# Kernel optimization log

Hardware: AMD Instinct MI355X
Metric: run time of the kernel (lower is better)

The kernel has to match this reference:

```python
import jax, jax.numpy as jnp
import numpy as np

NUM_ITER = 5
ALPHA = 5.0   # spatial bandwidth, bilateral kernel
BETA = 5.0    # feature bandwidth, bilateral kernel
GAMMA = 5.0   # spatial bandwidth, spatial kernel
W_1 = 1.0
W_2 = 1.0


def setup_inputs() -> dict:
    key = jax.random.key(0)
    k1, k2 = jax.random.split(key)
    B, C, X, Y, Z = 1, 4, 32, 16, 16
    log_unary = jax.random.normal(k1, (B, C, X, Y, Z), dtype=jnp.float32)
    features_pairwise = jax.random.normal(k2, (B, 2, X, Y, Z), dtype=jnp.float32)
    # Potts-model compatibility: ones minus identity, [C_out, C_in] (conv1d kernel size 1)
    compatibility_weights = (jnp.ones((C, C)) - jnp.eye(C)).astype(jnp.float32)
    return {"log_unary": log_unary, "features_pairwise": features_pairwise,
            "compatibility_weights": compatibility_weights}


def _gauss_kernel(f):
    # f: [B, D, N] feature vectors; dense Gaussian filter matrix K_ij = exp(-||f_i-f_j||^2/2)
    sq = jnp.sum(f * f, axis=1)  # [B, N]
    d2 = sq[:, :, None] + sq[:, None, :] - 2.0 * jnp.einsum('bdn,bdm->bnm', f, f)
    return jnp.exp(-0.5 * jnp.maximum(d2, 0.0))  # [B, N, N]


def reference(log_unary, features_pairwise, compatibility_weights):
    B, C, X, Y, Z = log_unary.shape
    N = X * Y * Z
    lu = log_unary.reshape(B, C, N)
    q = jax.nn.softmax(lu, axis=1)

    gx, gy, gz = jnp.meshgrid(jnp.arange(X), jnp.arange(Y), jnp.arange(Z), indexing='ij')
    spatial = jnp.stack([gx, gy, gz], axis=0).astype(jnp.float32).reshape(1, 3, N)
    spatial = jnp.broadcast_to(spatial, (B, 3, N))
    img_fea = features_pairwise.reshape(B, features_pairwise.shape[1], N)

    f1 = jnp.concatenate([spatial / ALPHA, img_fea / BETA], axis=1)  # bilateral features
    f2 = spatial / GAMMA                                             # spatial features

    K1 = _gauss_kernel(f1)
    K2 = _gauss_kernel(f2)
    # norm = filter(ones) = row sums; scale = rsqrt(norm)
    scale1 = jax.lax.rsqrt(jnp.sum(K1, axis=2))[:, None, :]  # [B,1,N]
    scale2 = jax.lax.rsqrt(jnp.sum(K2, axis=2))[:, None, :]

    for _ in range(NUM_ITER):
        q1 = jnp.einsum('bnm,bcm->bcn', K1, q * scale1) * scale1
        q2 = jnp.einsum('bnm,bcm->bcn', K2, q * scale2) * scale2
        q_comb = W_1 * q1 + W_2 * q2
        q_update = jnp.einsum('oc,bcn->bon', compatibility_weights, q_comb)
        q = jax.nn.softmax(lu - q_update, axis=1)

    return q.reshape(B, C, X, Y, Z)
```

## Files before the change

### kernel.cpp

```cpp
#include <hip/hip_runtime.h>
#include <math.h>


constexpr int   NT    = 8192;
constexpr float SQL2E = 1.2011224087864498f;
constexpr float LOG2E = 1.4426950408889634f;
constexpr float INVA  = 0.2f * SQL2E;

constexpr int R_M = 0, R_U1 = 32, R_U2 = 36, R_S1 = 40, R_S2 = 41, R_CV = 42;

static __device__ __forceinline__ float ex2(float x) {
    return __builtin_amdgcn_exp2f(x);
}

__constant__ float INVSQF[7] = {1.f, 1.f, 0.70710678f, 0.40824829f,
                                0.20412415f, 0.09128709f, 0.03726780f};

__global__ __launch_bounds__(256) void k_setup(const float* __restrict__ feat,
                                               float* __restrict__ W) {
    int n = blockIdx.x * 256 + threadIdx.x;
    float g0 = feat[n] * 0.2f, g1 = feat[NT + n] * 0.2f;
    float eg = ex2(-0.5f * LOG2E * (g0*g0 + g1*g1));
    float p0[7], p1[7];
    p0[0] = 1.f; p1[0] = 1.f;
#pragma unroll
    for (int i = 1; i < 7; i++) { p0[i] = p0[i-1]*g0; p1[i] = p1[i-1]*g1; }
    int ab = 0;
#pragma unroll
    for (int k = 0; k <= 6; k++)
#pragma unroll
        for (int a = k; a >= 0; a--) {
            int b = k - a;
            W[(R_M + ab)*NT + n] = eg * p0[a]*INVSQF[a] * p1[b]*INVSQF[b];
            ab++;
        }
    int x = n >> 8, y = (n >> 4) & 15, z = n & 15;
    float Sx = 0.f, Sy = 0.f, Sz = 0.f;
    for (int j = 0; j < 32; j++) { float d = (float)(x-j)*INVA; Sx += ex2(-0.5f*d*d); }
    for (int j = 0; j < 16; j++) { float d = (float)(y-j)*INVA; Sy += ex2(-0.5f*d*d); }
    for (int j = 0; j < 16; j++) { float d = (float)(z-j)*INVA; Sz += ex2(-0.5f*d*d); }
    W[R_S2*NT + n] = rsqrtf(Sx * Sy * Sz);
}

__global__ __launch_bounds__(256) void k_conv(const float* __restrict__ W,
                                              float* __restrict__ Wout, int mode) {
    __shared__ float SP[512 * 17];
    const int idx = blockIdx.x;
    const int tid = threadIdx.x;
    if (mode == 0) {
        const float* src = W + (R_M + idx) * NT;
        for (int s = tid; s < NT; s += 256)
            SP[(s >> 4)*17 + (s & 15)] = src[s];
    } else if (idx < 112) {
        const float* Mr = W + (R_M + (idx >> 2)) * NT;
        const float* ur = W + (R_U1 + (idx & 3)) * NT;
        for (int s = tid; s < NT; s += 256)
            SP[(s >> 4)*17 + (s & 15)] = Mr[s] * ur[s];
    } else {
        const float* ur = W + (R_U2 + (idx - 112)) * NT;
        for (int s = tid; s < NT; s += 256)
            SP[(s >> 4)*17 + (s & 15)] = ur[s];
    }
    float g32[32];
#pragma unroll
    for (int d = 0; d < 32; d++) { float t = d * INVA; g32[d] = ex2(-0.5f*t*t); }
    __syncthreads();
#pragma unroll
    for (int rr = 0; rr < 2; rr++) {
        int r = tid + rr * 256;
        float v[16], acc[16];
#pragma unroll
        for (int z = 0; z < 16; z++) { v[z] = SP[r*17 + z]; acc[z] = 0.f; }
#pragma unroll
        for (int zp = 0; zp < 16; zp++)
#pragma unroll
            for (int z = 0; z < 16; z++) {
                int d = (z > zp) ? (z - zp) : (zp - z);
                acc[z] = fmaf(g32[d], v[zp], acc[z]);
            }
#pragma unroll
        for (int z = 0; z < 16; z++) SP[r*17 + z] = acc[z];
    }
    __syncthreads();
#pragma unroll
    for (int rr = 0; rr < 2; rr++) {
        int r = tid + rr * 256;
        int x = r >> 4, z = r & 15;
        int base = x * 272 + z;
        float v[16], acc[16];
#pragma unroll
        for (int y = 0; y < 16; y++) { v[y] = SP[base + y*17]; acc[y] = 0.f; }
#pragma unroll
        for (int yp = 0; yp < 16; yp++)
#pragma unroll
            for (int y = 0; y < 16; y++) {
                int d = (y > yp) ? (y - yp) : (yp - y);
                acc[y] = fmaf(g32[d], v[yp], acc[y]);
            }
#pragma unroll
        for (int y = 0; y < 16; y++) SP[base + y*17] = acc[y];
    }
    __syncthreads();
    {
        int base = (tid >> 4) * 17 + (tid & 15);
        float v[32], acc[32];
#pragma unroll
        for (int xp = 0; xp < 32; xp++) { v[xp] = SP[base + xp*272]; acc[xp] = 0.f; }
#pragma unroll
        for (int xp = 0; xp < 32; xp++)
#pragma unroll
            for (int x = 0; x < 32; x++) {
                int d = (x > xp) ? (x - xp) : (xp - x);
                acc[x] = fmaf(g32[d], v[xp], acc[x]);
            }
        float* outp = Wout + (R_CV + idx) * NT;
#pragma unroll
        for (int x = 0; x < 32; x++) outp[x*256 + tid] = acc[x];
    }
}

__global__ __launch_bounds__(256) void k_init(float* __restrict__ W,
                                              const float* __restrict__ lu) {
    int n = blockIdx.x * 256 + threadIdx.x;
    float rs = 0.f;
#pragma unroll
    for (int ab = 0; ab < 28; ab++)
        rs = fmaf(W[(R_M+ab)*NT + n], W[(R_CV+ab)*NT + n], rs);
    float s1 = rsqrtf(rs);
    float s2 = W[R_S2*NT + n];
    W[R_S1*NT + n] = s1;
    float l0 = lu[n], l1 = lu[NT+n], l2 = lu[2*NT+n], l3 = lu[3*NT+n];
    float mx = fmaxf(fmaxf(l0,l1), fmaxf(l2,l3));
    float q0 = __expf(l0-mx), q1 = __expf(l1-mx), q2 = __expf(l2-mx), q3 = __expf(l3-mx);
    float inv = 1.f / (q0+q1+q2+q3);
    q0*=inv; q1*=inv; q2*=inv; q3*=inv;
    W[(R_U1+0)*NT+n]=q0*s1; W[(R_U1+1)*NT+n]=q1*s1; W[(R_U1+2)*NT+n]=q2*s1; W[(R_U1+3)*NT+n]=q3*s1;
    W[(R_U2+0)*NT+n]=q0*s2; W[(R_U2+1)*NT+n]=q1*s2; W[(R_U2+2)*NT+n]=q2*s2; W[(R_U2+3)*NT+n]=q3*s2;
}

__global__ __launch_bounds__(256) void k_fuse(float* __restrict__ W,
        const float* __restrict__ lu, const float* __restrict__ compat,
        float* __restrict__ out) {
    int n = blockIdx.x * 256 + threadIdx.x;
    float s1 = W[R_S1*NT + n], s2 = W[R_S2*NT + n];
    float q1[4] = {0.f, 0.f, 0.f, 0.f};
#pragma unroll
    for (int ab = 0; ab < 28; ab++) {
        float m = W[(R_M+ab)*NT + n];
#pragma unroll
        for (int c = 0; c < 4; c++)
            q1[c] = fmaf(m, W[(R_CV + ab*4 + c)*NT + n], q1[c]);
    }
    float comb[4];
#pragma unroll
    for (int c = 0; c < 4; c++)
        comb[c] = s1 * q1[c] + s2 * W[(R_CV + 112 + c)*NT + n];
    float q[4];
#pragma unroll
    for (int o = 0; o < 4; o++) {
        float upd = 0.f;
#pragma unroll
        for (int c = 0; c < 4; c++) upd = fmaf(compat[o*4+c], comb[c], upd);
        q[o] = lu[o*NT+n] - upd;
    }
    float mx = fmaxf(fmaxf(q[0],q[1]), fmaxf(q[2],q[3]));
    float sum = 0.f;
#pragma unroll
    for (int c = 0; c < 4; c++) { q[c] = __expf(q[c]-mx); sum += q[c]; }
    float inv = 1.f / sum;
#pragma unroll
    for (int c = 0; c < 4; c++) {
        q[c] *= inv;
        out[c*NT+n]        = q[c];
        W[(R_U1+c)*NT+n]   = q[c]*s1;
        W[(R_U2+c)*NT+n]   = q[c]*s2;
    }
}

extern "C" void kernel_launch(void* const* d_in, const int* in_sizes, int n_in,
                              void* d_out, int out_size, void* d_ws, size_t ws_size,
                              hipStream_t stream) {
    const float* lu     = (const float*)d_in[0];
    const float* feat   = (const float*)d_in[1];
    const float* compat = (const float*)d_in[2];
    float* out = (float*)d_out;
    float* W   = (float*)d_ws;

    k_setup<<<dim3(32), dim3(256), 0, stream>>>(feat, W);
    k_conv <<<dim3(28), dim3(256), 0, stream>>>(W, W, 0);
    k_init <<<dim3(32), dim3(256), 0, stream>>>(W, lu);
    for (int it = 0; it < 5; it++) {
        k_conv<<<dim3(116), dim3(256), 0, stream>>>(W, W, 1);
        k_fuse<<<dim3(32),  dim3(256), 0, stream>>>(W, lu, compat, out);
    }
}
```

Before: 147.2 us.

## Fuse all stages into one persistent kernel with atomic grid barriers

Replaces the thirteen separate kernel launches (setup, initial conv, init, then conv+fuse per iteration) with a single persistent kernel of 116 blocks that synchronises stages through an atomic-counter grid barrier. Setup is folded into the first conv stage by computing the moment channels directly into shared memory, and the final iteration skips writing the scaled q buffers. This is meant to remove per-launch overhead and inter-kernel gaps. In exchange it adds a memset launch, spin-wait barriers that depend on all 116 blocks being co-resident, and extra atomic latency at each stage boundary.

```diff
diff --git a/kernel.cpp b/kernel.cpp
--- a/kernel.cpp
+++ b/kernel.cpp
@@ -3,68 +3,35 @@
 
 
 constexpr int   NT    = 8192;
+constexpr int   NB    = 116;
 constexpr float SQL2E = 1.2011224087864498f;
 constexpr float LOG2E = 1.4426950408889634f;
 constexpr float INVA  = 0.2f * SQL2E;
 
-constexpr int R_M = 0, R_U1 = 32, R_U2 = 36, R_S1 = 40, R_S2 = 41, R_CV = 42;
+constexpr int R_M = 0, R_S1 = 28, R_S2 = 29, R_U1 = 30, R_U2 = 34, R_CV = 38;
+constexpr int R_CNT = 154;
+
+__constant__ float INVSQF[7] = {1.f, 1.f, 0.70710678f, 0.40824829f,
+                                0.20412415f, 0.09128709f, 0.03726780f};
 
 static __device__ __forceinline__ float ex2(float x) {
     return __builtin_amdgcn_exp2f(x);
 }
 
-__constant__ float INVSQF[7] = {1.f, 1.f, 0.70710678f, 0.40824829f,
-                                0.20412415f, 0.09128709f, 0.03726780f};
-
-__global__ __launch_bounds__(256) void k_setup(const float* __restrict__ feat,
-                                               float* __restrict__ W) {
-    int n = blockIdx.x * 256 + threadIdx.x;
-    float g0 = feat[n] * 0.2f, g1 = feat[NT + n] * 0.2f;
-    float eg = ex2(-0.5f * LOG2E * (g0*g0 + g1*g1));
-    float p0[7], p1[7];
-    p0[0] = 1.f; p1[0] = 1.f;
-#pragma unroll
-    for (int i = 1; i < 7; i++) { p0[i] = p0[i-1]*g0; p1[i] = p1[i-1]*g1; }
-    int ab = 0;
-#pragma unroll
-    for (int k = 0; k <= 6; k++)
-#pragma unroll
-        for (int a = k; a >= 0; a--) {
-            int b = k - a;
-            W[(R_M + ab)*NT + n] = eg * p0[a]*INVSQF[a] * p1[b]*INVSQF[b];
-            ab++;
-        }
-    int x = n >> 8, y = (n >> 4) & 15, z = n & 15;
-    float Sx = 0.f, Sy = 0.f, Sz = 0.f;
-    for (int j = 0; j < 32; j++) { float d = (float)(x-j)*INVA; Sx += ex2(-0.5f*d*d); }
-    for (int j = 0; j < 16; j++) { float d = (float)(y-j)*INVA; Sy += ex2(-0.5f*d*d); }
-    for (int j = 0; j < 16; j++) { float d = (float)(z-j)*INVA; Sz += ex2(-0.5f*d*d); }
-    W[R_S2*NT + n] = rsqrtf(Sx * Sy * Sz);
-}
-
-__global__ __launch_bounds__(256) void k_conv(const float* __restrict__ W,
-                                              float* __restrict__ Wout, int mode) {
-    __shared__ float SP[512 * 17];
-    const int idx = blockIdx.x;
-    const int tid = threadIdx.x;
-    if (mode == 0) {
-        const float* src = W + (R_M + idx) * NT;
-        for (int s = tid; s < NT; s += 256)
-            SP[(s >> 4)*17 + (s & 15)] = src[s];
-    } else if (idx < 112) {
-        const float* Mr = W + (R_M + (idx >> 2)) * NT;
-        const float* ur = W + (R_U1 + (idx & 3)) * NT;
-        for (int s = tid; s < NT; s += 256)
-            SP[(s >> 4)*17 + (s & 15)] = Mr[s] * ur[s];
-    } else {
-        const float* ur = W + (R_U2 + (idx - 112)) * NT;
-        for (int s = tid; s < NT; s += 256)
-            SP[(s >> 4)*17 + (s & 15)] = ur[s];
-    }
-    float g32[32];
-#pragma unroll
-    for (int d = 0; d < 32; d++) { float t = d * INVA; g32[d] = ex2(-0.5f*t*t); }
-    __syncthreads();
+static __device__ __forceinline__ void gridbar(unsigned* cnt, unsigned target) {
+    __syncthreads();
+    if (threadIdx.x == 0) {
+        __threadfence();
+        atomicAdd(cnt, 1u);
+        while (__hip_atomic_load(cnt, __ATOMIC_ACQUIRE, __HIP_MEMORY_SCOPE_AGENT) < target)
+            __builtin_amdgcn_s_sleep(1);
+        __threadfence();
+    }
+    __syncthreads();
+}
+
+static __device__ __forceinline__ void conv3d(float* SP, const float* g32,
+                                              float* __restrict__ outp, int tid) {
 #pragma unroll
     for (int rr = 0; rr < 2; rr++) {
         int r = tid + rr * 256;
@@ -85,8 +52,7 @@
 #pragma unroll
     for (int rr = 0; rr < 2; rr++) {
         int r = tid + rr * 256;
-        int x = r >> 4, z = r & 15;
-        int base = x * 272 + z;
+        int base = (r >> 4) * 272 + (r & 15);
         float v[16], acc[16];
 #pragma unroll
         for (int y = 0; y < 16; y++) { v[y] = SP[base + y*17]; acc[y] = 0.f; }
@@ -113,67 +79,122 @@
                 int d = (x > xp) ? (x - xp) : (xp - x);
                 acc[x] = fmaf(g32[d], v[xp], acc[x]);
             }
-        float* outp = Wout + (R_CV + idx) * NT;
 #pragma unroll
         for (int x = 0; x < 32; x++) outp[x*256 + tid] = acc[x];
     }
 }
 
-__global__ __launch_bounds__(256) void k_init(float* __restrict__ W,
-                                              const float* __restrict__ lu) {
-    int n = blockIdx.x * 256 + threadIdx.x;
-    float rs = 0.f;
-#pragma unroll
-    for (int ab = 0; ab < 28; ab++)
-        rs = fmaf(W[(R_M+ab)*NT + n], W[(R_CV+ab)*NT + n], rs);
-    float s1 = rsqrtf(rs);
-    float s2 = W[R_S2*NT + n];
-    W[R_S1*NT + n] = s1;
-    float l0 = lu[n], l1 = lu[NT+n], l2 = lu[2*NT+n], l3 = lu[3*NT+n];
-    float mx = fmaxf(fmaxf(l0,l1), fmaxf(l2,l3));
-    float q0 = __expf(l0-mx), q1 = __expf(l1-mx), q2 = __expf(l2-mx), q3 = __expf(l3-mx);
-    float inv = 1.f / (q0+q1+q2+q3);
-    q0*=inv; q1*=inv; q2*=inv; q3*=inv;
-    W[(R_U1+0)*NT+n]=q0*s1; W[(R_U1+1)*NT+n]=q1*s1; W[(R_U1+2)*NT+n]=q2*s1; W[(R_U1+3)*NT+n]=q3*s1;
-    W[(R_U2+0)*NT+n]=q0*s2; W[(R_U2+1)*NT+n]=q1*s2; W[(R_U2+2)*NT+n]=q2*s2; W[(R_U2+3)*NT+n]=q3*s2;
-}
-
-__global__ __launch_bounds__(256) void k_fuse(float* __restrict__ W,
-        const float* __restrict__ lu, const float* __restrict__ compat,
-        float* __restrict__ out) {
-    int n = blockIdx.x * 256 + threadIdx.x;
-    float s1 = W[R_S1*NT + n], s2 = W[R_S2*NT + n];
-    float q1[4] = {0.f, 0.f, 0.f, 0.f};
-#pragma unroll
-    for (int ab = 0; ab < 28; ab++) {
-        float m = W[(R_M+ab)*NT + n];
-#pragma unroll
-        for (int c = 0; c < 4; c++)
-            q1[c] = fmaf(m, W[(R_CV + ab*4 + c)*NT + n], q1[c]);
-    }
-    float comb[4];
-#pragma unroll
-    for (int c = 0; c < 4; c++)
-        comb[c] = s1 * q1[c] + s2 * W[(R_CV + 112 + c)*NT + n];
-    float q[4];
-#pragma unroll
-    for (int o = 0; o < 4; o++) {
-        float upd = 0.f;
-#pragma unroll
-        for (int c = 0; c < 4; c++) upd = fmaf(compat[o*4+c], comb[c], upd);
-        q[o] = lu[o*NT+n] - upd;
-    }
-    float mx = fmaxf(fmaxf(q[0],q[1]), fmaxf(q[2],q[3]));
-    float sum = 0.f;
-#pragma unroll
-    for (int c = 0; c < 4; c++) { q[c] = __expf(q[c]-mx); sum += q[c]; }
-    float inv = 1.f / sum;
-#pragma unroll
-    for (int c = 0; c < 4; c++) {
-        q[c] *= inv;
-        out[c*NT+n]        = q[c];
-        W[(R_U1+c)*NT+n]   = q[c]*s1;
-        W[(R_U2+c)*NT+n]   = q[c]*s2;
+__global__ __launch_bounds__(256) void k_mega(const float* __restrict__ lu,
+        const float* __restrict__ feat, const float* __restrict__ compat,
+        float* __restrict__ out, float* __restrict__ W) {
+    __shared__ float SP[512 * 17];
+    const int bid = blockIdx.x, tid = threadIdx.x;
+    unsigned* cnt = (unsigned*)(W + (size_t)R_CNT * NT);
+    unsigned bar = 0;
+    float g32[32];
+#pragma unroll
+    for (int d = 0; d < 32; d++) { float t = d * INVA; g32[d] = ex2(-0.5f*t*t); }
+
+    if (bid < 28) {
+        int a = 0, b = 0;
+        { int r = bid;
+          for (int k = 0; k <= 6; k++) { if (r <= k) { a = k - r; b = r; break; } r -= k + 1; } }
+        float cN = INVSQF[a] * INVSQF[b];
+        for (int s = tid; s < NT; s += 256) {
+            float g0 = feat[s] * 0.2f, g1 = feat[NT + s] * 0.2f;
+            float eg = ex2(-0.5f * LOG2E * (g0*g0 + g1*g1));
+            float pa = 1.f;
+            for (int i = 0; i < a; i++) pa *= g0;
+            float pb = 1.f;
+            for (int i = 0; i < b; i++) pb *= g1;
+            float val = eg * pa * pb * cN;
+            W[(R_M + bid)*NT + s] = val;
+            SP[(s >> 4)*17 + (s & 15)] = val;
+        }
+        __syncthreads();
+        conv3d(SP, g32, W + (size_t)(R_CV + bid)*NT, tid);
+    }
+    bar += NB; gridbar(cnt, bar);
+
+    {
+        int n = bid * 256 + tid;
+        if (n < NT) {
+            float rs = 0.f;
+#pragma unroll
+            for (int ab = 0; ab < 28; ab++)
+                rs = fmaf(W[(R_M+ab)*NT + n], W[(R_CV+ab)*NT + n], rs);
+            float s1 = rsqrtf(rs);
+            int x = n >> 8, y = (n >> 4) & 15, z = n & 15;
+            float Sx = 0.f, Sy = 0.f, Sz = 0.f;
+            for (int j = 0; j < 32; j++) { float d = (float)(x-j)*INVA; Sx += ex2(-0.5f*d*d); }
+            for (int j = 0; j < 16; j++) { float d = (float)(y-j)*INVA; Sy += ex2(-0.5f*d*d); }
+            for (int j = 0; j < 16; j++) { float d = (float)(z-j)*INVA; Sz += ex2(-0.5f*d*d); }
+            float s2 = rsqrtf(Sx * Sy * Sz);
+            W[R_S1*NT+n] = s1; W[R_S2*NT+n] = s2;
+            float l0 = lu[n], l1 = lu[NT+n], l2 = lu[2*NT+n], l3 = lu[3*NT+n];
+            float mx = fmaxf(fmaxf(l0,l1), fmaxf(l2,l3));
+            float q0 = __expf(l0-mx), q1 = __expf(l1-mx), q2 = __expf(l2-mx), q3 = __expf(l3-mx);
+            float inv = 1.f / (q0+q1+q2+q3);
+            q0*=inv; q1*=inv; q2*=inv; q3*=inv;
+            W[(R_U1+0)*NT+n]=q0*s1; W[(R_U1+1)*NT+n]=q1*s1; W[(R_U1+2)*NT+n]=q2*s1; W[(R_U1+3)*NT+n]=q3*s1;
+            W[(R_U2+0)*NT+n]=q0*s2; W[(R_U2+1)*NT+n]=q1*s2; W[(R_U2+2)*NT+n]=q2*s2; W[(R_U2+3)*NT+n]=q3*s2;
+        }
+    }
+
+    for (int it = 0; it < 5; it++) {
+        bar += NB; gridbar(cnt, bar);
+        if (bid < 112) {
+            const float* Mr = W + (size_t)(R_M  + (bid >> 2)) * NT;
+            const float* ur = W + (size_t)(R_U1 + (bid & 3)) * NT;
+            for (int s = tid; s < NT; s += 256)
+                SP[(s >> 4)*17 + (s & 15)] = Mr[s] * ur[s];
+        } else {
+            const float* ur = W + (size_t)(R_U2 + (bid - 112)) * NT;
+            for (int s = tid; s < NT; s += 256)
+                SP[(s >> 4)*17 + (s & 15)] = ur[s];
+        }
+        __syncthreads();
+        conv3d(SP, g32, W + (size_t)(R_CV + bid)*NT, tid);
+        bar += NB; gridbar(cnt, bar);
+
+        int n = bid * 256 + tid;
+        if (n < NT) {
+            float s1 = W[R_S1*NT+n], s2 = W[R_S2*NT+n];
+            float y1[4] = {0.f, 0.f, 0.f, 0.f};
+#pragma unroll
+            for (int ab = 0; ab < 28; ab++) {
+                float m = W[(R_M+ab)*NT + n];
+#pragma unroll
+                for (int c = 0; c < 4; c++)
+                    y1[c] = fmaf(m, W[(R_CV + ab*4 + c)*NT + n], y1[c]);
+            }
+            float comb[4], q[4];
+#pragma unroll
+            for (int c = 0; c < 4; c++)
+                comb[c] = s1 * y1[c] + s2 * W[(R_CV + 112 + c)*NT + n];
+#pragma unroll
+            for (int o = 0; o < 4; o++) {
+                float upd = 0.f;
+#pragma unroll
+                for (int c = 0; c < 4; c++) upd = fmaf(compat[o*4+c], comb[c], upd);
+                q[o] = lu[o*NT+n] - upd;
+            }
+            float mx = fmaxf(fmaxf(q[0],q[1]), fmaxf(q[2],q[3]));
+            float sum = 0.f;
+#pragma unroll
+            for (int c = 0; c < 4; c++) { q[c] = __expf(q[c]-mx); sum += q[c]; }
+            float inv = 1.f / sum;
+#pragma unroll
+            for (int c = 0; c < 4; c++) {
+                q[c] *= inv;
+                if (it == 4) {
+                    out[c*NT+n] = q[c];
+                } else {
+                    W[(R_U1+c)*NT+n] = q[c]*s1;
+                    W[(R_U2+c)*NT+n] = q[c]*s2;
+                }
+            }
+        }
     }
 }
 
@@ -186,11 +207,6 @@
     float* out = (float*)d_out;
     float* W   = (float*)d_ws;
 
-    k_setup<<<dim3(32), dim3(256), 0, stream>>>(feat, W);
-    k_conv <<<dim3(28), dim3(256), 0, stream>>>(W, W, 0);
-    k_init <<<dim3(32), dim3(256), 0, stream>>>(W, lu);
-    for (int it = 0; it < 5; it++) {
-        k_conv<<<dim3(116), dim3(256), 0, stream>>>(W, W, 1);
-        k_fuse<<<dim3(32),  dim3(256), 0, stream>>>(W, lu, compat, out);
-    }
-}
+    hipMemsetAsync((char*)d_ws + (size_t)R_CNT * NT * sizeof(float), 0, 64, stream);
+    k_mega<<<dim3(NB), dim3(256), 0, stream>>>(lu, feat, compat, out, W);
+}
```

Result: slower. 574.5 us (+290.2%).
